# Performance work log

Hardware: AMD Instinct MI355X
Metric: run time of the kernel (lower is better)

Reference implementation:

```python
import jax, jax.numpy as jnp
import numpy as np

DYN_CH = 16   # dyn_ch
MASK_CH = 16  # mask_ch (use_low_level_info=True -> num_bases=16)
UP_F = 8      # upsample_f
POUT = 256    # pad_out_channel


def _conv(x, w, padding):
    # NCHW conv, stride 1
    return jax.lax.conv_general_dilated(x, w, (1, 1), padding,
                                        dimension_numbers=('NCHW', 'OIHW', 'NCHW'))


def _bn(x, scale, shift):
    # inference-mode (Sync)BatchNorm folded to affine: scale=gamma/sqrt(var+eps), shift=beta-mean*scale
    return x * scale[None, :, None, None] + shift[None, :, None, None]


def _padconv(x, w, b, cin, cout, relu):
    # Faithful math of padconv(repeat -> mul -> grouped ones-conv -> bias -> relu),
    # expressed as a per-pixel dynamic 1x1 conv. Since w/b are nearest-upsampled
    # from HxW by factor f, we contract at low resolution per fxf block instead of
    # materializing the cout*cin-channel repeated tensors.
    # x: [B, cin, H*f, W*f]; w: [B, cout*cin, H, W]; b: [B, cout, H, W]
    B, _, Hf, Wf = x.shape
    H, W = w.shape[2], w.shape[3]
    f = Hf // H
    xb = x.reshape(B, cin, H, f, W, f)
    wr = w.reshape(B, cout, cin, H, W)
    out = jnp.einsum('bchpwq,bochw->bohpwq', xb, wr) + b[:, :, :, None, :, None]
    out = out.reshape(B, cout, Hf, Wf)
    return jax.nn.relu(out) if relu else out


def setup_inputs() -> dict:
    key = jax.random.key(0)
    ks = jax.random.split(key, 8)
    B, H, W = 8, 16, 16
    f = UP_F
    num_out = (2 + 16) * 16 + 16 + 16 * 16 + 16 + 16 * 256 + 256  # 4928
    inp = {}
    inp['res5'] = jax.random.normal(ks[0], (B, 2048, H, W), jnp.float32)
    inp['res2'] = jax.random.normal(ks[1], (B, 256, H * f, W * f), jnp.float32)
    inp['bottleneck_w'] = jax.random.normal(ks[2], (512, 2048, 3, 3), jnp.float32) * 0.01
    inp['bn1_scale'] = jnp.ones((512,), jnp.float32)
    inp['bn1_shift'] = jnp.zeros((512,), jnp.float32)
    inp['cls0_w'] = jax.random.normal(ks[3], (1024, 1024, 3, 3), jnp.float32) * 0.01
    inp['bn2_scale'] = jnp.ones((1024,), jnp.float32)
    inp['bn2_shift'] = jnp.zeros((1024,), jnp.float32)
    inp['cls1_w'] = jax.random.normal(ks[4], (num_out, 1024, 1, 1), jnp.float32) * 0.01
    inp['cls1_b'] = jnp.zeros((num_out,), jnp.float32)
    inp['c1a_w'] = jax.random.normal(ks[5], (48, 256, 3, 3), jnp.float32) * 0.02
    inp['bn3_scale'] = jnp.ones((48,), jnp.float32)
    inp['bn3_shift'] = jnp.zeros((48,), jnp.float32)
    inp['c1b_w'] = jax.random.normal(ks[6], (16, 48, 1, 1), jnp.float32) * 0.05
    inp['c1b_b'] = jnp.zeros((16,), jnp.float32)
    inp['cat_scale'] = jnp.ones((18,), jnp.float32)
    inp['cat_shift'] = jnp.zeros((18,), jnp.float32)
    return inp


def reference(res5, res2, bottleneck_w, bn1_scale, bn1_shift, cls0_w, bn2_scale,
              bn2_shift, cls1_w, cls1_b, c1a_w, bn3_scale, bn3_shift, c1b_w,
              c1b_b, cat_scale, cat_shift):
    B, _, H, W = res5.shape
    f = UP_F
    # bottleneck: conv3x3 -> BN -> relu
    x = jax.nn.relu(_bn(_conv(res5, bottleneck_w, 'SAME'), bn1_scale, bn1_shift))
    # global image pool, broadcast back, concat
    gp = jnp.broadcast_to(jnp.mean(x, axis=(2, 3), keepdims=True), x.shape)
    x = jnp.concatenate([x, gp], axis=1)
    # classifier: conv3x3 -> BN -> relu -> conv1x1 (+bias) => hyper-network params
    x = jax.nn.relu(_bn(_conv(x, cls0_w, 'SAME'), bn2_scale, bn2_shift))
    x = _conv(x, cls1_w, 'VALID') + cls1_b[None, :, None, None]  # [B, 4928, H, W]
    # c1_bottleneck on res2 (low-level features at H*f x W*f)
    c1 = jax.nn.relu(_bn(_conv(res2, c1a_w, 'SAME'), bn3_scale, bn3_shift))
    c1 = _conv(c1, c1b_w, 'VALID') + c1b_b[None, :, None, None]  # [B, 16, H*f, W*f]
    # split hyper-net output into per-pixel MLP weights/biases
    ch, nb = DYN_CH, MASK_CH
    sizes = [(2 + nb) * ch, ch, ch * ch, ch, ch * POUT, POUT]
    splits = np.cumsum(sizes)[:-1].tolist()
    w0, b0, w1, b1, w2, b2 = jnp.split(x, splits, axis=1)
    # coord grid: per fxf block, (x, y) in [0,1), tiled over HxW blocks
    xs = jnp.arange(f, dtype=jnp.float32) / f
    gy, gx = jnp.meshgrid(xs, xs, indexing='ij')
    loc = jnp.stack([gx, gy], axis=0)               # [2, f, f]
    coord = jnp.tile(loc, (1, H, W))                # [2, H*f, W*f]
    coord = jnp.broadcast_to(coord[None], (B, 2, H * f, W * f))
    inp = _bn(jnp.concatenate([coord, c1], axis=1), cat_scale, cat_shift)  # cat_norm
    # 3-layer per-pixel dynamic MLP (padconv trick, fused here)
    h = _padconv(inp, w0, b0, 2 + nb, ch, True)
    h = _padconv(h, w1, b1, ch, ch, True)
    out = _padconv(h, w2, b2, ch, POUT, False)      # [B, 256, H*f, W*f]
    return out
```

## Files before the change

kernel.cpp:

```cpp
#include <hip/hip_runtime.h>

#define B8 8

typedef __attribute__((ext_vector_type(8))) short short8;
typedef __attribute__((ext_vector_type(4))) float floatx4;

static __device__ __forceinline__ unsigned short f2bf(float f) {
  unsigned int u = __float_as_uint(f);
  unsigned int r = (u + 0x7fffu + ((u >> 16) & 1u)) >> 16;
  return (unsigned short)r;
}

__global__ __launch_bounds__(256) void wtransform(
    const float* __restrict__ w, unsigned short* __restrict__ wT,
    int Cout, int Cin)
{
  int idx = blockIdx.x * 256 + threadIdx.x;
  if (idx >= Cout * Cin) return;
  int ci = idx % Cin, co = idx / Cin;
  const float* s = w + (size_t)idx * 9;
#pragma unroll
  for (int t = 0; t < 9; ++t)
    wT[((size_t)t * Cout + co) * Cin + ci] = f2bf(s[t]);
}

__global__ __launch_bounds__(256) void cvt_bf16(
    const float* __restrict__ w, unsigned short* __restrict__ o, int n)
{
  int i = blockIdx.x * 256 + threadIdx.x;
  if (i < n) o[i] = f2bf(w[i]);
}

__global__ __launch_bounds__(256) void nchw2nhwc_bf16(
    const float* __restrict__ in, unsigned short* __restrict__ out)
{
  int t = blockIdx.x;
  int pb = t & 63;
  int cb = (t >> 6) & 7;
  int b = t >> 9;

  __shared__ unsigned short sT[32][260];

  int tid = threadIdx.x;
  int c4 = tid >> 6;
  int px4 = (tid & 63) << 2;

  const float* ip = in + ((size_t)(b * 256 + cb * 32) * 16384) + pb * 256;
#pragma unroll
  for (int cc = 0; cc < 8; ++cc) {
    int ci = cc * 4 + c4;
    float4 v = *(const float4*)&ip[(size_t)ci * 16384 + px4];
    unsigned int p0 = (unsigned)f2bf(v.x) | ((unsigned)f2bf(v.y) << 16);
    unsigned int p1 = (unsigned)f2bf(v.z) | ((unsigned)f2bf(v.w) << 16);
    *(unsigned int*)&sT[ci][px4] = p0;
    *(unsigned int*)&sT[ci][px4 + 2] = p1;
  }
  __syncthreads();

  int px = tid;
  unsigned short* op =
      out + ((size_t)(b * 16384 + pb * 256 + px) * 256) + cb * 32;
#pragma unroll
  for (int j = 0; j < 4; ++j) {
    short8 o;
#pragma unroll
    for (int k = 0; k < 8; ++k) o[k] = (short)sT[j * 8 + k][px];
    *(short8*)&op[j * 8] = o;
  }
}

__global__ __launch_bounds__(256, 2) void conv3x3_hi_nhwc(
    const unsigned short* __restrict__ xh,
    const unsigned short* __restrict__ wT,
    const float* __restrict__ scale, const float* __restrict__ shift,
    const float* __restrict__ w1,
    const float* __restrict__ b1,
    float* __restrict__ c1)
{
  int t = blockIdx.x;
  int tile = t & 63;
  int b = t >> 6;
  int ty0 = (tile >> 3) << 4, tx0 = (tile & 7) << 4;

  __shared__ float sW1[16 * 48];
  __shared__ float sB1[16];

  int tid = threadIdx.x;
  for (int i = tid; i < 768; i += 256) sW1[i] = w1[i];
  if (tid < 16) sB1[tid] = b1[tid];
  __syncthreads();

  int lane = tid & 63, w = tid >> 6;
  int l15 = lane & 15, q = lane >> 4;

  const unsigned short* xb = xh + (size_t)b * 16384 * 256 + q * 8;
  int ofs[6][3];
  bool vv[6][3];
#pragma unroll
  for (int rr = 0; rr < 6; ++rr) {
    int gy = ty0 + w * 4 - 1 + rr;
#pragma unroll
    for (int cc = 0; cc < 3; ++cc) {
      int gx = tx0 + l15 - 1 + cc;
      bool v = (unsigned)gy < 128u && (unsigned)gx < 128u;
      vv[rr][cc] = v;
      ofs[rr][cc] = v ? ((gy * 128 + gx) * 256) : 0;
    }
  }

  floatx4 acc[3][4];
#pragma unroll
  for (int ct = 0; ct < 3; ++ct)
#pragma unroll
    for (int pt = 0; pt < 4; ++pt) acc[ct][pt] = (floatx4){0.f, 0.f, 0.f, 0.f};

  const short8 z8 = (short8){0, 0, 0, 0, 0, 0, 0, 0};

  for (int ci0 = 0; ci0 < 256; ci0 += 32) {
    short8 pix[6][3];
#pragma unroll
    for (int rr = 0; rr < 6; ++rr)
#pragma unroll
      for (int cc = 0; cc < 3; ++cc)
        pix[rr][cc] =
            vv[rr][cc] ? *(const short8*)&xb[ofs[rr][cc] + ci0] : z8;
#pragma unroll
    for (int ky = 0; ky < 3; ++ky) {
#pragma unroll
      for (int kx = 0; kx < 3; ++kx) {
        int tap = ky * 3 + kx;
        const unsigned short* wbase =
            wT + ((size_t)(tap * 48 + l15)) * 256 + ci0 + q * 8;
        short8 af[3];
#pragma unroll
        for (int ct = 0; ct < 3; ++ct)
          af[ct] = *(const short8*)(wbase + ct * 16 * 256);
#pragma unroll
        for (int ct = 0; ct < 3; ++ct)
#pragma unroll
          for (int pt = 0; pt < 4; ++pt)
            acc[ct][pt] = __builtin_amdgcn_mfma_f32_16x16x32_bf16(
                af[ct], pix[pt + ky][kx], acc[ct][pt], 0, 0, 0);
      }
    }
  }

#pragma unroll
  for (int ct = 0; ct < 3; ++ct) {
#pragma unroll
    for (int r = 0; r < 4; ++r) {
      int c = ct * 16 + q * 4 + r;
      float sc = scale[c], sh = shift[c];
#pragma unroll
      for (int pt = 0; pt < 4; ++pt) {
        float x = fmaf(acc[ct][pt][r], sc, sh);
        acc[ct][pt][r] = x > 0.0f ? x : 0.0f;
      }
    }
  }

  float* cp = c1 + (size_t)b * 16 * 16384 + (size_t)ty0 * 128 + tx0 + l15;
#pragma unroll
  for (int co = 0; co < 16; ++co) {
    float wv[12];
#pragma unroll
    for (int ct = 0; ct < 3; ++ct)
#pragma unroll
      for (int r = 0; r < 4; ++r)
        wv[ct * 4 + r] = sW1[co * 48 + ct * 16 + q * 4 + r];
    float s[4];
#pragma unroll
    for (int pt = 0; pt < 4; ++pt) {
      float a = 0.0f;
#pragma unroll
      for (int ct = 0; ct < 3; ++ct)
#pragma unroll
        for (int r = 0; r < 4; ++r)
          a = fmaf(wv[ct * 4 + r], acc[ct][pt][r], a);
      a += __shfl_xor(a, 16, 64);
      a += __shfl_xor(a, 32, 64);
      s[pt] = a;
    }
    if (q == (co >> 2)) {
      float bb = sB1[co];
#pragma unroll
      for (int pt = 0; pt < 4; ++pt)
        cp[(size_t)co * 16384 + (w * 4 + pt) * 128] = s[pt] + bb;
    }
  }
}

__global__ __launch_bounds__(256, 2) void conv3x3_mfma(
    const void* __restrict__ inv,
    const unsigned short* __restrict__ wT,
    float* __restrict__ part, int Cin, int Cout, int nCoBlk, int nSlice,
    int inBf16)
{
  int t = blockIdx.x;
  int slice = t % nSlice; t /= nSlice;
  int ph = t & 1; t >>= 1;
  int cb = t % nCoBlk; t /= nCoBlk;
  int b = t;
  int ciSlice = Cin / nSlice;
  int nTiles = ciSlice >> 5;

  __shared__ unsigned short sIn[10 * 18 * 40];

  int tid = threadIdx.x;
  int lane = tid & 63, wave = tid >> 6;
  int wc = wave >> 1, wp = wave & 1;
  int l15 = lane & 15, q = lane >> 4;

  for (int i = tid; i < (10 * 18 * 40) / 2; i += 256) ((unsigned int*)sIn)[i] = 0u;

  floatx4 acc[4][4];
#pragma unroll
  for (int ct = 0; ct < 4; ++ct)
#pragma unroll
    for (int pt = 0; pt < 4; ++pt) acc[ct][pt] = (floatx4){0.f, 0.f, 0.f, 0.f};

  int coBase = cb * 128 + wc * 64;
  int gr0 = ph * 7;
  int sr0 = 1 - ph;

  int gofs[18], lofs[18];
#pragma unroll
  for (int k = 0; k < 18; ++k) {
    int i = tid + k * 256;
    int px = i & 15, r9 = i >> 4;
    int rr = r9 % 9, ci = r9 / 9;
    gofs[k] = ci * 256 + (gr0 + rr) * 16 + px;
    lofs[k] = ((sr0 + rr) * 18 + 1 + px) * 40 + ci;
  }
  const float* inbF = (const float*)inv + (size_t)b * Cin * 256;
  const unsigned short* inbU = (const unsigned short*)inv + (size_t)b * Cin * 256;

  unsigned int pf[18];
  {
    int ci0 = slice * ciSlice;
    if (inBf16) {
#pragma unroll
      for (int k = 0; k < 18; ++k) pf[k] = inbU[(size_t)ci0 * 256 + gofs[k]];
    } else {
#pragma unroll
      for (int k = 0; k < 18; ++k)
        pf[k] = __float_as_uint(inbF[(size_t)ci0 * 256 + gofs[k]]);
    }
  }

  for (int ct2 = 0; ct2 < nTiles; ++ct2) {
    int ci0 = slice * ciSlice + ct2 * 32;
    __syncthreads();
    if (inBf16) {
#pragma unroll
      for (int k = 0; k < 18; ++k) sIn[lofs[k]] = (unsigned short)pf[k];
    } else {
#pragma unroll
      for (int k = 0; k < 18; ++k) sIn[lofs[k]] = f2bf(__uint_as_float(pf[k]));
    }
    __syncthreads();
    if (ct2 + 1 < nTiles) {
      int cin0 = ci0 + 32;
      if (inBf16) {
#pragma unroll
        for (int k = 0; k < 18; ++k) pf[k] = inbU[(size_t)cin0 * 256 + gofs[k]];
      } else {
#pragma unroll
        for (int k = 0; k < 18; ++k)
          pf[k] = __float_as_uint(inbF[(size_t)cin0 * 256 + gofs[k]]);
      }
    }
#pragma unroll
    for (int ky = 0; ky < 3; ++ky) {
#pragma unroll
      for (int kx = 0; kx < 3; ++kx) {
        int tap = ky * 3 + kx;
        const unsigned short* wbase =
            wT + ((size_t)(tap * Cout + coBase + l15)) * Cin + ci0 + q * 8;
        short8 af[4];
#pragma unroll
        for (int ct = 0; ct < 4; ++ct)
          af[ct] = *(const short8*)(wbase + (size_t)ct * 16 * Cin);
        short8 bf[4];
#pragma unroll
        for (int pt = 0; pt < 4; ++pt) {
          int sRow = wp * 4 + pt + ky;
          int sCol = l15 + kx;
          bf[pt] = *(const short8*)&sIn[(sRow * 18 + sCol) * 40 + q * 8];
        }
#pragma unroll
        for (int ct = 0; ct < 4; ++ct)
#pragma unroll
          for (int pt = 0; pt < 4; ++pt)
            acc[ct][pt] = __builtin_amdgcn_mfma_f32_16x16x32_bf16(
                af[ct], bf[pt], acc[ct][pt], 0, 0, 0);
      }
    }
  }

  float* po = part + ((size_t)(slice * B8 + b) * Cout) * 256;
#pragma unroll
  for (int ct = 0; ct < 4; ++ct) {
#pragma unroll
    for (int pt = 0; pt < 4; ++pt) {
      int co = coBase + ct * 16 + q * 4;
      int px = ph * 128 + wp * 64 + pt * 16 + l15;
#pragma unroll
      for (int r = 0; r < 4; ++r)
        po[(size_t)(co + r) * 256 + px] = acc[ct][pt][r];
    }
  }
}

__global__ __launch_bounds__(256) void combine1(
    const float* __restrict__ part, const float* __restrict__ scale,
    const float* __restrict__ shift, unsigned short* __restrict__ out,
    int Cout, int nSlice, int outStride)
{
  int c = blockIdx.x % Cout, b = blockIdx.x / Cout;
  int tid = threadIdx.x;
  float s = 0.0f;
  for (int sl = 0; sl < nSlice; ++sl)
    s += part[(((size_t)sl * B8 + b) * Cout + c) * 256 + tid];
  float v = fmaf(s, scale[c], shift[c]);
  v = v > 0.0f ? v : 0.0f;
  out[((size_t)b * outStride + c) * 256 + tid] = f2bf(v);
  __shared__ float red[4];
  float w = v;
#pragma unroll
  for (int off = 32; off > 0; off >>= 1) w += __shfl_down(w, off, 64);
  if ((tid & 63) == 0) red[tid >> 6] = w;
  __syncthreads();
  float m = (red[0] + red[1] + red[2] + red[3]) * (1.0f / 256.0f);
  out[((size_t)b * outStride + Cout + c) * 256 + tid] = f2bf(m);
}

__global__ __launch_bounds__(256) void combine2T(
    const float* __restrict__ part, const float* __restrict__ scale,
    const float* __restrict__ shift, unsigned short* __restrict__ x2T)
{
  int t = blockIdx.x;
  int cg = t & 3;
  int pxg = (t >> 2) & 15;
  int b = t >> 6;
  int c16 = threadIdx.x >> 4, px16 = threadIdx.x & 15;
  int px = pxg * 16 + px16;
#pragma unroll
  for (int k = 0; k < 4; ++k) {
    int cBase = cg * 256 + k * 64 + c16 * 4;
    unsigned short v4[4];
#pragma unroll
    for (int j = 0; j < 4; ++j) {
      int c = cBase + j;
      float s = 0.0f;
#pragma unroll
      for (int sl = 0; sl < 4; ++sl)
        s += part[(((size_t)sl * B8 + b) * 1024 + c) * 256 + px];
      float v = fmaf(s, scale[c], shift[c]);
      v4[j] = f2bf(v > 0.0f ? v : 0.0f);
    }
    *(ushort2*)&x2T[((size_t)b * 256 + px) * 1024 + cBase] =
        *(ushort2*)&v4[0];
    *(ushort2*)&x2T[((size_t)b * 256 + px) * 1024 + cBase + 2] =
        *(ushort2*)&v4[2];
  }
}

__global__ __launch_bounds__(256, 2) void hyper_gemm(
    const unsigned short* __restrict__ wH,
    const unsigned short* __restrict__ x2T,
    const float* __restrict__ bias,
    float* __restrict__ hyper)
{
  int cb = blockIdx.x % 77, b = blockIdx.x / 77;
  int tid = threadIdx.x;
  int lane = tid & 63, w = tid >> 6;
  int l15 = lane & 15, q = lane >> 4;

  floatx4 acc[4][4];
#pragma unroll
  for (int ct = 0; ct < 4; ++ct)
#pragma unroll
    for (int pt = 0; pt < 4; ++pt) acc[ct][pt] = (floatx4){0.f, 0.f, 0.f, 0.f};

  const unsigned short* wp0 = wH + ((size_t)(cb * 64 + l15)) * 1024 + q * 8;
  const unsigned short* xp0 =
      x2T + ((size_t)(b * 256 + w * 64 + l15)) * 1024 + q * 8;

  for (int ci0 = 0; ci0 < 1024; ci0 += 32) {
    short8 af[4], bf[4];
#pragma unroll
    for (int ct = 0; ct < 4; ++ct)
      af[ct] = *(const short8*)(wp0 + (size_t)ct * 16 * 1024 + ci0);
#pragma unroll
    for (int pt = 0; pt < 4; ++pt)
      bf[pt] = *(const short8*)(xp0 + (size_t)pt * 16 * 1024 + ci0);
#pragma unroll
    for (int ct = 0; ct < 4; ++ct)
#pragma unroll
      for (int pt = 0; pt < 4; ++pt)
        acc[ct][pt] = __builtin_amdgcn_mfma_f32_16x16x32_bf16(
            af[ct], bf[pt], acc[ct][pt], 0, 0, 0);
  }

#pragma unroll
  for (int ct = 0; ct < 4; ++ct) {
    int co = cb * 64 + ct * 16 + q * 4;
#pragma unroll
    for (int pt = 0; pt < 4; ++pt) {
      int px = w * 64 + pt * 16 + l15;
#pragma unroll
      for (int r = 0; r < 4; ++r)
        hyper[((size_t)b * 4928 + co + r) * 256 + px] = acc[ct][pt][r] + bias[co + r];
    }
  }
}

__global__ __launch_bounds__(256) void dyn_mlp(
    const float* __restrict__ hyper, const float* __restrict__ c1,
    const float* __restrict__ catS, const float* __restrict__ catB,
    float* __restrict__ out)
{
  int t = blockIdx.x;
  int q = t & 3;
  int h = (t >> 2) & 15;
  int b = t >> 6;
  int tid = threadIdx.x;
  int xf = tid & 127, r2 = tid >> 7;
  int w = xf >> 3;

  __shared__ float smem[16 * 578];
  __shared__ float sB2[16 * 33];

  const float* hypb = hyper + (size_t)b * 4928 * 256 + h * 16;

  for (int i = tid; i < 576 * 16; i += 256) {
    int ch = i >> 4, ww = i & 15;
    smem[ww * 578 + ch] = hypb[(size_t)ch * 256 + ww];
  }

  float cs[18], cb[18];
#pragma unroll
  for (int i = 0; i < 18; ++i) { cs[i] = catS[i]; cb[i] = catB[i]; }

  float inpv[4][18];
  int yf0 = h * 8 + r2 * 4;
  float cx = (float)(xf & 7) * 0.125f;
#pragma unroll
  for (int k = 0; k < 4; ++k) {
    inpv[k][0] = fmaf(cx, cs[0], cb[0]);
    inpv[k][1] = fmaf((float)((yf0 + k) & 7) * 0.125f, cs[1], cb[1]);
#pragma unroll
    for (int ci = 0; ci < 16; ++ci) {
      float v = c1[((size_t)b * 16 + ci) * 16384 + (size_t)(yf0 + k) * 128 + xf];
      inpv[k][2 + ci] = fmaf(v, cs[2 + ci], cb[2 + ci]);
    }
  }
  __syncthreads();

  const float* sw = smem + w * 578;
  float h0v[4][16];
  {
    const float2* w0p = (const float2*)sw;
#pragma unroll
    for (int co = 0; co < 16; ++co) {
      float a0 = sw[288 + co], a1 = a0, a2 = a0, a3 = a0;
#pragma unroll
      for (int c2 = 0; c2 < 9; ++c2) {
        float2 wv = w0p[co * 9 + c2];
        a0 = fmaf(wv.x, inpv[0][2 * c2], a0); a0 = fmaf(wv.y, inpv[0][2 * c2 + 1], a0);
        a1 = fmaf(wv.x, inpv[1][2 * c2], a1); a1 = fmaf(wv.y, inpv[1][2 * c2 + 1], a1);
        a2 = fmaf(wv.x, inpv[2][2 * c2], a2); a2 = fmaf(wv.y, inpv[2][2 * c2 + 1], a2);
        a3 = fmaf(wv.x, inpv[3][2 * c2], a3); a3 = fmaf(wv.y, inpv[3][2 * c2 + 1], a3);
      }
      h0v[0][co] = fmaxf(a0, 0.0f); h0v[1][co] = fmaxf(a1, 0.0f);
      h0v[2][co] = fmaxf(a2, 0.0f); h0v[3][co] = fmaxf(a3, 0.0f);
    }
  }
  float h1v[4][16];
  {
    const float2* w1p = (const float2*)(sw + 304);
#pragma unroll
    for (int co = 0; co < 16; ++co) {
      float a0 = sw[560 + co], a1 = a0, a2 = a0, a3 = a0;
#pragma unroll
      for (int c2 = 0; c2 < 8; ++c2) {
        float2 wv = w1p[co * 8 + c2];
        a0 = fmaf(wv.x, h0v[0][2 * c2], a0); a0 = fmaf(wv.y, h0v[0][2 * c2 + 1], a0);
        a1 = fmaf(wv.x, h0v[1][2 * c2], a1); a1 = fmaf(wv.y, h0v[1][2 * c2 + 1], a1);
        a2 = fmaf(wv.x, h0v[2][2 * c2], a2); a2 = fmaf(wv.y, h0v[2][2 * c2 + 1], a2);
        a3 = fmaf(wv.x, h0v[3][2 * c2], a3); a3 = fmaf(wv.y, h0v[3][2 * c2 + 1], a3);
      }
      h1v[0][co] = fmaxf(a0, 0.0f); h1v[1][co] = fmaxf(a1, 0.0f);
      h1v[2][co] = fmaxf(a2, 0.0f); h1v[3][co] = fmaxf(a3, 0.0f);
    }
  }

  for (int chunk = 0; chunk < 2; ++chunk) {
    int po0 = q * 64 + chunk * 32;
    __syncthreads();
    for (int i = tid; i < 8192; i += 256) {
      int ch = i >> 4, ww = i & 15;
      smem[ww * 518 + ch] = hypb[(size_t)(576 + po0 * 16 + ch) * 256 + ww];
    }
    for (int i = tid; i < 512; i += 256) {
      int po = i >> 4, ww = i & 15;
      sB2[ww * 33 + po] = hypb[(size_t)(4672 + po0 + po) * 256 + ww];
    }
    __syncthreads();
    const float2* w2p = (const float2*)(smem + w * 518);
    const float* sb2 = sB2 + w * 33;
#pragma unroll 4
    for (int po = 0; po < 32; ++po) {
      float a0 = sb2[po], a1 = a0, a2 = a0, a3 = a0;
#pragma unroll
      for (int c2 = 0; c2 < 8; ++c2) {
        float2 wv = w2p[po * 8 + c2];
        a0 = fmaf(wv.x, h1v[0][2 * c2], a0); a0 = fmaf(wv.y, h1v[0][2 * c2 + 1], a0);
        a1 = fmaf(wv.x, h1v[1][2 * c2], a1); a1 = fmaf(wv.y, h1v[1][2 * c2 + 1], a1);
        a2 = fmaf(wv.x, h1v[2][2 * c2], a2); a2 = fmaf(wv.y, h1v[2][2 * c2 + 1], a2);
        a3 = fmaf(wv.x, h1v[3][2 * c2], a3); a3 = fmaf(wv.y, h1v[3][2 * c2 + 1], a3);
      }
      size_t ob = ((size_t)b * 256 + po0 + po) * 16384 + (size_t)yf0 * 128 + xf;
      out[ob] = a0; out[ob + 128] = a1; out[ob + 256] = a2; out[ob + 384] = a3;
    }
  }
}

extern "C" void kernel_launch(void* const* d_in, const int* in_sizes, int n_in,
                              void* d_out, int out_size, void* d_ws, size_t ws_size,
                              hipStream_t stream) {
  const float* res5 = (const float*)d_in[0];
  const float* res2 = (const float*)d_in[1];
  const float* bw   = (const float*)d_in[2];
  const float* bn1s = (const float*)d_in[3];
  const float* bn1b = (const float*)d_in[4];
  const float* c0w  = (const float*)d_in[5];
  const float* bn2s = (const float*)d_in[6];
  const float* bn2b = (const float*)d_in[7];
  const float* cls1w = (const float*)d_in[8];
  const float* cls1b = (const float*)d_in[9];
  const float* c1aw = (const float*)d_in[10];
  const float* bn3s = (const float*)d_in[11];
  const float* bn3b = (const float*)d_in[12];
  const float* c1bw = (const float*)d_in[13];
  const float* c1bb = (const float*)d_in[14];
  const float* catS = (const float*)d_in[15];
  const float* catB = (const float*)d_in[16];
  float* out = (float*)d_out;
  float* ws = (float*)d_ws;

  unsigned short* wT2u  = (unsigned short*)(ws);
  float* c1             = ws;
  unsigned short* wT48  = (unsigned short*)(ws + 2097152);
  unsigned short* x2cat = (unsigned short*)(ws + 4718592);
  unsigned short* x2T   = (unsigned short*)(ws + 5767168);
  float* hyper          = ws + 6815744;
  unsigned short* wT1u  = (unsigned short*)(ws + 6815744);
  float* partial        = ws + 16908288;
  unsigned short* wH    = (unsigned short*)(ws + 16908288);
  unsigned short* x2nhwc = (unsigned short*)(ws + 16908288);

  wtransform<<<(512 * 2048 + 255) / 256, 256, 0, stream>>>(bw, wT1u, 512, 2048);
  wtransform<<<(1024 * 1024 + 255) / 256, 256, 0, stream>>>(c0w, wT2u, 1024, 1024);
  conv3x3_mfma<<<8 * 4 * 2 * 8, 256, 0, stream>>>(res5, wT1u, partial, 2048, 512, 4, 8, 0);
  combine1<<<8 * 512, 256, 0, stream>>>(partial, bn1s, bn1b, x2cat, 512, 8, 1024);
  conv3x3_mfma<<<8 * 8 * 2 * 4, 256, 0, stream>>>(x2cat, wT2u, partial, 1024, 1024, 8, 4, 1);
  combine2T<<<8 * 16 * 4, 256, 0, stream>>>(partial, bn2s, bn2b, x2T);
  cvt_bf16<<<(4928 * 1024 + 255) / 256, 256, 0, stream>>>(cls1w, wH, 4928 * 1024);
  hyper_gemm<<<77 * 8, 256, 0, stream>>>(wH, x2T, cls1b, hyper);

  wtransform<<<(48 * 256 + 255) / 256, 256, 0, stream>>>(c1aw, wT48, 48, 256);
  for (int half = 0; half < 2; ++half) {
    nchw2nhwc_bf16<<<4 * 8 * 64, 256, 0, stream>>>(
        res2 + (size_t)half * 4 * 256 * 16384, x2nhwc);
    conv3x3_hi_nhwc<<<4 * 64, 256, 0, stream>>>(
        x2nhwc, wT48, bn3s, bn3b, c1bw, c1bb,
        c1 + (size_t)half * 4 * 16 * 16384);
  }

  dyn_mlp<<<8 * 16 * 4, 256, 0, stream>>>(hyper, c1, catS, catB, out);
}
```

Before: 760.8 us.

## Shrink hyper GEMM tile with register double-buffering; batch low-level conv in one pass

The hyper-network GEMM now uses 32-channel tiles with twice as many blocks and higher occupancy. Its K-loop is software-pipelined so the next operand fragments load while the current MFMAs run. The res2 layout transform and low-level conv now run once over the full batch instead of two halves, and are scheduled first. This needs a larger, reorganised workspace. The aim is to hide global-load latency and cut launch overhead, at the cost of more register pressure and less operand reuse per block.

```diff
diff --git a/kernel.cpp b/kernel.cpp
--- a/kernel.cpp
+++ b/kernel.cpp
@@ -366,46 +366,67 @@
   }
 }
 
-__global__ __launch_bounds__(256, 2) void hyper_gemm(
+__global__ __launch_bounds__(256, 4) void hyper_gemm(
     const unsigned short* __restrict__ wH,
     const unsigned short* __restrict__ x2T,
     const float* __restrict__ bias,
     float* __restrict__ hyper)
 {
-  int cb = blockIdx.x % 77, b = blockIdx.x / 77;
+  int cb = blockIdx.x % 154, b = blockIdx.x / 154;
   int tid = threadIdx.x;
   int lane = tid & 63, w = tid >> 6;
   int l15 = lane & 15, q = lane >> 4;
 
-  floatx4 acc[4][4];
-#pragma unroll
-  for (int ct = 0; ct < 4; ++ct)
+  floatx4 acc[2][4];
+#pragma unroll
+  for (int ct = 0; ct < 2; ++ct)
 #pragma unroll
     for (int pt = 0; pt < 4; ++pt) acc[ct][pt] = (floatx4){0.f, 0.f, 0.f, 0.f};
 
-  const unsigned short* wp0 = wH + ((size_t)(cb * 64 + l15)) * 1024 + q * 8;
+  const unsigned short* wp0 = wH + ((size_t)(cb * 32 + l15)) * 1024 + q * 8;
   const unsigned short* xp0 =
       x2T + ((size_t)(b * 256 + w * 64 + l15)) * 1024 + q * 8;
 
-  for (int ci0 = 0; ci0 < 1024; ci0 += 32) {
-    short8 af[4], bf[4];
-#pragma unroll
-    for (int ct = 0; ct < 4; ++ct)
-      af[ct] = *(const short8*)(wp0 + (size_t)ct * 16 * 1024 + ci0);
+  short8 a0[2], b0[4], a1[2], b1[4];
+#pragma unroll
+  for (int ct = 0; ct < 2; ++ct)
+    a0[ct] = *(const short8*)(wp0 + ct * 16 * 1024);
+#pragma unroll
+  for (int pt = 0; pt < 4; ++pt)
+    b0[pt] = *(const short8*)(xp0 + pt * 16 * 1024);
+
+  for (int ci0 = 0; ci0 < 1024; ci0 += 64) {
+#pragma unroll
+    for (int ct = 0; ct < 2; ++ct)
+      a1[ct] = *(const short8*)(wp0 + ct * 16 * 1024 + ci0 + 32);
 #pragma unroll
     for (int pt = 0; pt < 4; ++pt)
-      bf[pt] = *(const short8*)(xp0 + (size_t)pt * 16 * 1024 + ci0);
-#pragma unroll
-    for (int ct = 0; ct < 4; ++ct)
+      b1[pt] = *(const short8*)(xp0 + pt * 16 * 1024 + ci0 + 32);
+#pragma unroll
+    for (int ct = 0; ct < 2; ++ct)
 #pragma unroll
       for (int pt = 0; pt < 4; ++pt)
         acc[ct][pt] = __builtin_amdgcn_mfma_f32_16x16x32_bf16(
-            af[ct], bf[pt], acc[ct][pt], 0, 0, 0);
-  }
-
-#pragma unroll
-  for (int ct = 0; ct < 4; ++ct) {
-    int co = cb * 64 + ct * 16 + q * 4;
+            a0[ct], b0[pt], acc[ct][pt], 0, 0, 0);
+    if (ci0 + 64 < 1024) {
+#pragma unroll
+      for (int ct = 0; ct < 2; ++ct)
+        a0[ct] = *(const short8*)(wp0 + ct * 16 * 1024 + ci0 + 64);
+#pragma unroll
+      for (int pt = 0; pt < 4; ++pt)
+        b0[pt] = *(const short8*)(xp0 + pt * 16 * 1024 + ci0 + 64);
+    }
+#pragma unroll
+    for (int ct = 0; ct < 2; ++ct)
+#pragma unroll
+      for (int pt = 0; pt < 4; ++pt)
+        acc[ct][pt] = __builtin_amdgcn_mfma_f32_16x16x32_bf16(
+            a1[ct], b1[pt], acc[ct][pt], 0, 0, 0);
+  }
+
+#pragma unroll
+  for (int ct = 0; ct < 2; ++ct) {
+    int co = cb * 32 + ct * 16 + q * 4;
 #pragma unroll
     for (int pt = 0; pt < 4; ++pt) {
       int px = w * 64 + pt * 16 + l15;
@@ -550,16 +571,21 @@
   float* out = (float*)d_out;
   float* ws = (float*)d_ws;
 
-  unsigned short* wT2u  = (unsigned short*)(ws);
-  float* c1             = ws;
-  unsigned short* wT48  = (unsigned short*)(ws + 2097152);
-  unsigned short* x2cat = (unsigned short*)(ws + 4718592);
-  unsigned short* x2T   = (unsigned short*)(ws + 5767168);
-  float* hyper          = ws + 6815744;
-  unsigned short* wT1u  = (unsigned short*)(ws + 6815744);
-  float* partial        = ws + 16908288;
-  unsigned short* wH    = (unsigned short*)(ws + 16908288);
-  unsigned short* x2nhwc = (unsigned short*)(ws + 16908288);
+  float* c1              = ws;
+  unsigned short* x2nhwc = (unsigned short*)(ws + 2097152);
+  unsigned short* wT48   = (unsigned short*)(ws + 24543232);
+  unsigned short* wT1u   = (unsigned short*)(ws + 2097152);
+  float* partial         = ws + 6815744;
+  unsigned short* x2cat  = (unsigned short*)(ws + 15204352);
+  unsigned short* wT2u   = (unsigned short*)(ws + 16252928);
+  unsigned short* x2T    = (unsigned short*)(ws + 20971520);
+  unsigned short* wH     = (unsigned short*)(ws + 22020096);
+  float* hyper           = ws + 6815744;
+
+  wtransform<<<(48 * 256 + 255) / 256, 256, 0, stream>>>(c1aw, wT48, 48, 256);
+  nchw2nhwc_bf16<<<8 * 8 * 64, 256, 0, stream>>>(res2, x2nhwc);
+  conv3x3_hi_nhwc<<<8 * 64, 256, 0, stream>>>(x2nhwc, wT48, bn3s, bn3b,
+                                              c1bw, c1bb, c1);
 
   wtransform<<<(512 * 2048 + 255) / 256, 256, 0, stream>>>(bw, wT1u, 512, 2048);
   wtransform<<<(1024 * 1024 + 255) / 256, 256, 0, stream>>>(c0w, wT2u, 1024, 1024);
@@ -568,16 +594,7 @@
   conv3x3_mfma<<<8 * 8 * 2 * 4, 256, 0, stream>>>(x2cat, wT2u, partial, 1024, 1024, 8, 4, 1);
   combine2T<<<8 * 16 * 4, 256, 0, stream>>>(partial, bn2s, bn2b, x2T);
   cvt_bf16<<<(4928 * 1024 + 255) / 256, 256, 0, stream>>>(cls1w, wH, 4928 * 1024);
-  hyper_gemm<<<77 * 8, 256, 0, stream>>>(wH, x2T, cls1b, hyper);
-
-  wtransform<<<(48 * 256 + 255) / 256, 256, 0, stream>>>(c1aw, wT48, 48, 256);
-  for (int half = 0; half < 2; ++half) {
-    nchw2nhwc_bf16<<<4 * 8 * 64, 256, 0, stream>>>(
-        res2 + (size_t)half * 4 * 256 * 16384, x2nhwc);
-    conv3x3_hi_nhwc<<<4 * 64, 256, 0, stream>>>(
-        x2nhwc, wT48, bn3s, bn3b, c1bw, c1bb,
-        c1 + (size_t)half * 4 * 16 * 16384);
-  }
+  hyper_gemm<<<154 * 8, 256, 0, stream>>>(wH, x2T, cls1b, hyper);
 
   dyn_mlp<<<8 * 16 * 4, 256, 0, stream>>>(hyper, c1, catS, catB, out);
 }
```

Result: no change. 762.7 us (+0.3%).
